# Kernel tuning notes

Measured on AMD Instinct MI355X. Metric: run time of the kernel, lower is better.

Reference implementation:

```python
import jax, jax.numpy as jnp
import numpy as np

D_MODEL = 1024
D_INNER = 2048   # expand * d_model
D_STATE = 16
D_CONV = 4
DT_RANK = 64     # ceil(d_model / 16)
BATCH = 2
SEQLEN = 4096


def setup_inputs() -> dict:
    key = jax.random.key(0)
    ks = jax.random.split(key, 9)
    g = lambda k, shape, scale: jax.random.normal(k, shape, dtype=jnp.float32) * scale
    hidden_states = g(ks[0], (BATCH, SEQLEN, D_MODEL), 1.0)
    W_in = g(ks[1], (2 * D_INNER, D_MODEL), D_MODEL ** -0.5)
    conv_w = g(ks[2], (D_INNER, D_CONV), D_CONV ** -0.5)
    conv_b = g(ks[3], (D_INNER,), 0.02)
    x_proj_w = g(ks[4], (DT_RANK + 2 * D_STATE, D_INNER), D_INNER ** -0.5)
    dt_w = g(ks[5], (D_INNER, DT_RANK), DT_RANK ** -0.5)
    # dt bias init as in Mamba: inverse softplus of dt ~ U[log(1e-3), log(1e-1)]
    dt = jnp.exp(jax.random.uniform(ks[6], (D_INNER,), dtype=jnp.float32)
                 * (np.log(0.1) - np.log(0.001)) + np.log(0.001))
    dt = jnp.clip(dt, 1e-4, None)
    dt_b = dt + jnp.log(-jnp.expm1(-dt))
    # A_log init: log of [1..d_state] repeated per channel
    A_log = jnp.log(jnp.tile(jnp.arange(1, D_STATE + 1, dtype=jnp.float32), (D_INNER, 1)))
    D = jnp.ones((D_INNER,), dtype=jnp.float32)
    W_out = g(ks[7], (D_MODEL, D_INNER), D_INNER ** -0.5)
    return dict(hidden_states=hidden_states, W_in=W_in, conv_w=conv_w, conv_b=conv_b,
                x_proj_w=x_proj_w, dt_w=dt_w, dt_b=dt_b, A_log=A_log, D=D, W_out=W_out)


def reference(hidden_states, W_in, conv_w, conv_b, x_proj_w, dt_w, dt_b, A_log, D, W_out):
    B, L, _ = hidden_states.shape
    # in_proj + transpose -> (B, 2*Din, L)
    xz = jnp.einsum('bld,ed->bel', hidden_states, W_in)
    # nanotron (tp=1) splits via view(B, d_inner, 2, L): interleaved channels
    xz = xz.reshape(B, D_INNER, 2, L)
    x, z = xz[:, :, 0, :], xz[:, :, 1, :]          # (B, Din, L)
    # causal depthwise conv1d (pad left d_conv-1) + SiLU
    xc = jax.lax.conv_general_dilated(
        x, conv_w[:, None, :], window_strides=(1,), padding=[(D_CONV - 1, 0)],
        dimension_numbers=('NCH', 'OIH', 'NCH'), feature_group_count=D_INNER)
    x = jax.nn.silu(xc + conv_b[None, :, None])     # (B, Din, L)
    # x_proj -> dt, B, C
    x_dbl = jnp.einsum('bdl,ed->ble', x, x_proj_w)  # (B, L, dt_rank+2N)
    dt, Bm, Cm = jnp.split(x_dbl, [DT_RANK, DT_RANK + D_STATE], axis=-1)
    delta = jnp.einsum('blr,dr->bdl', dt, dt_w)     # (B, Din, L)
    delta = jax.nn.softplus(delta + dt_b[None, :, None])
    A = -jnp.exp(A_log)                             # (Din, N)
    # selective scan over time
    xs = (jnp.transpose(delta, (2, 0, 1)),          # (L, B, Din)
          jnp.transpose(x, (2, 0, 1)),              # (L, B, Din)
          jnp.transpose(Bm, (1, 0, 2)),             # (L, B, N)
          jnp.transpose(Cm, (1, 0, 2)))             # (L, B, N)

    def step(s, inp):
        d_t, x_t, B_t, C_t = inp
        s = s * jnp.exp(d_t[:, :, None] * A[None]) + (d_t * x_t)[:, :, None] * B_t[:, None, :]
        y_t = jnp.einsum('bdn,bn->bd', s, C_t)
        return s, y_t

    s0 = jnp.zeros((B, D_INNER, D_STATE), dtype=hidden_states.dtype)
    _, ys = jax.lax.scan(step, s0, xs)              # ys: (L, B, Din)
    y = jnp.transpose(ys, (1, 2, 0))                # (B, Din, L)
    y = y + D[None, :, None] * x
    y = y * jax.nn.silu(z)
    out = jnp.einsum('bdl,md->blm', y, W_out)       # (B, L, d_model)
    return out
```

## Files before the change

kernel.cpp:

```cpp
#include <hip/hip_runtime.h>
#include <hip/hip_bf16.h>

#define D_MODEL 1024
#define D_INNER 2048
#define D_STATE 16
#define DT_RANK 64
#define BATCH 2
#define SEQLEN 4096
#define BL (BATCH * SEQLEN)
#define NPROJ (DT_RANK + 2 * D_STATE)
#define CH 64
#define NCH (SEQLEN / CH)

typedef __attribute__((ext_vector_type(8))) short bf16x8;
typedef __attribute__((ext_vector_type(4))) float f32x4;
struct S4 { short x, y, z, w; };

__device__ __forceinline__ float sigmoidf_(float v) {
    return 1.0f / (1.0f + __expf(-v));
}

__device__ __forceinline__ unsigned short bf16_rne(float f) {
    unsigned u = __float_as_uint(f);
    unsigned r = u + 0x7FFFu + ((u >> 16) & 1u);
    return (unsigned short)(r >> 16);
}

__device__ __forceinline__ float bf2f(short s) {
    return __uint_as_float(((unsigned)(unsigned short)s) << 16);
}

__global__ __launch_bounds__(256)
void cvt_split(const float* __restrict__ in, short* __restrict__ hi,
               short* __restrict__ lo, int n4) {
    const int i = blockIdx.x * 256 + threadIdx.x;
    if (i >= n4) return;
    const float4 v = reinterpret_cast<const float4*>(in)[i];
    const float f[4] = {v.x, v.y, v.z, v.w};
    S4 h, l;
    short hb[4], lb[4];
#pragma unroll
    for (int j = 0; j < 4; ++j) {
        const unsigned short hh = bf16_rne(f[j]);
        const float hf = __uint_as_float((unsigned)hh << 16);
        hb[j] = (short)hh;
        lb[j] = (short)bf16_rne(f[j] - hf);
    }
    h.x = hb[0]; h.y = hb[1]; h.z = hb[2]; h.w = hb[3];
    l.x = lb[0]; l.y = lb[1]; l.z = lb[2]; l.w = lb[3];
    *reinterpret_cast<S4*>(hi + (size_t)i * 4) = h;
    *reinterpret_cast<S4*>(lo + (size_t)i * 4) = l;
}

template <int EPI>
__global__ __launch_bounds__(256)
void gemm_bf16x3(const short* __restrict__ Ahi, const short* __restrict__ Alo,
                 const short* __restrict__ Bhi, const short* __restrict__ Blo,
                 float* __restrict__ C, int K, int lda, int ldb, int ldc,
                 const float* __restrict__ bias) {
    __shared__ short sA[2][2][128][32];
    __shared__ short sB[2][2][128][32];
    const int t = threadIdx.x;
    const int w = t >> 6, l = t & 63;

    const int nwg = gridDim.x * gridDim.y;
    int bid = blockIdx.y * gridDim.x + blockIdx.x;
    if ((nwg & 7) == 0) bid = (bid & 7) * (nwg >> 3) + (bid >> 3);
    const int m0 = (bid / gridDim.x) * 128, n0 = (bid % gridDim.x) * 128;
    const int wr = w >> 1, wc = w & 1;

    const short* gsrc;
    short* sd0;
    short* sd1;
    int ld, tile0;
    if (w == 0)      { gsrc = Ahi; sd0 = &sA[0][0][0][0]; sd1 = &sA[1][0][0][0]; tile0 = m0; ld = lda; }
    else if (w == 1) { gsrc = Alo; sd0 = &sA[0][1][0][0]; sd1 = &sA[1][1][0][0]; tile0 = m0; ld = lda; }
    else if (w == 2) { gsrc = Bhi; sd0 = &sB[0][0][0][0]; sd1 = &sB[1][0][0][0]; tile0 = n0; ld = ldb; }
    else             { gsrc = Blo; sd0 = &sB[0][1][0][0]; sd1 = &sB[1][1][0][0]; tile0 = n0; ld = ldb; }
    const int kc_src = ((l & 3) ^ ((l >> 3) & 3)) << 3;
    const size_t grow = (size_t)(tile0 + (l >> 2)) * ld + kc_src;

    f32x4 acc[4][4] = {};
    const int frow = l & 15;
    const int kb = (((l >> 4) ^ ((frow >> 1) & 3)) << 3);

    auto STAGE = [&](short* sdst, int k0) {
#pragma unroll
        for (int i = 0; i < 8; ++i) {
            const short* g = gsrc + grow + (size_t)(i << 4) * ld + k0;
            __builtin_amdgcn_global_load_lds(
                (const __attribute__((address_space(1))) void*)g,
                (__attribute__((address_space(3))) void*)(sdst + (i << 9)),
                16, 0, 0);
        }
    };

    auto COMPUTE = [&](int cur) {
        bf16x8 a[2][4], b[2][4];
#pragma unroll
        for (int f = 0; f < 4; ++f) {
            a[0][f] = *reinterpret_cast<const bf16x8*>(&sA[cur][0][wr * 64 + f * 16 + frow][kb]);
            a[1][f] = *reinterpret_cast<const bf16x8*>(&sA[cur][1][wr * 64 + f * 16 + frow][kb]);
            b[0][f] = *reinterpret_cast<const bf16x8*>(&sB[cur][0][wc * 64 + f * 16 + frow][kb]);
            b[1][f] = *reinterpret_cast<const bf16x8*>(&sB[cur][1][wc * 64 + f * 16 + frow][kb]);
        }
#pragma unroll
        for (int fi = 0; fi < 4; ++fi)
#pragma unroll
            for (int fj = 0; fj < 4; ++fj) {
                acc[fi][fj] = __builtin_amdgcn_mfma_f32_16x16x32_bf16(
                    a[0][fi], b[0][fj], acc[fi][fj], 0, 0, 0);
                acc[fi][fj] = __builtin_amdgcn_mfma_f32_16x16x32_bf16(
                    a[1][fi], b[0][fj], acc[fi][fj], 0, 0, 0);
                acc[fi][fj] = __builtin_amdgcn_mfma_f32_16x16x32_bf16(
                    a[0][fi], b[1][fj], acc[fi][fj], 0, 0, 0);
            }
    };

    const int NT = K >> 5;
    STAGE(sd0, 0);
    for (int tt = 0; tt < NT - 1; ++tt) {
        const int cur = tt & 1;
        STAGE(cur ? sd0 : sd1, (tt + 1) << 5);
        __builtin_amdgcn_sched_barrier(0);
        asm volatile("s_waitcnt vmcnt(8)" ::: "memory");
        __builtin_amdgcn_s_barrier();
        COMPUTE(cur);
        __builtin_amdgcn_sched_barrier(0);
        __builtin_amdgcn_s_barrier();
    }
    {
        const int cur = (NT - 1) & 1;
        __builtin_amdgcn_sched_barrier(0);
        asm volatile("s_waitcnt vmcnt(0)" ::: "memory");
        __builtin_amdgcn_s_barrier();
        COMPUTE(cur);
    }

    const int crow = (l >> 4) << 2;
    const int ccol = l & 15;
#pragma unroll
    for (int fi = 0; fi < 4; ++fi)
#pragma unroll
        for (int fj = 0; fj < 4; ++fj) {
            const int n = n0 + wc * 64 + fj * 16 + ccol;
#pragma unroll
            for (int r = 0; r < 4; ++r) {
                float v = acc[fi][fj][r];
                if (EPI == 1) {
                    v += bias[n];
                    v = fmaxf(v, 0.f) + log1pf(__expf(-fabsf(v)));
                }
                C[(size_t)(m0 + wr * 64 + fi * 16 + crow + r) * ldc + n] = v;
            }
        }
}

__global__ __launch_bounds__(256)
void gemm96(const short* __restrict__ Xhi, const short* __restrict__ Xlo,
            const short* __restrict__ Whi, const short* __restrict__ Wlo,
            float* __restrict__ C, short* __restrict__ dthi,
            short* __restrict__ dtlo) {
    const int t = threadIdx.x;
    const int w = t >> 6, l = t & 63;
    const int m0 = blockIdx.x * 32;
    const int rfrag = (w >> 1) * 16;
    const int cbase = (w & 1) * 48;
    const int lrow = l & 15;
    const int koff0 = (l >> 4) << 3;
    f32x4 acc[3] = {};
    const size_t arow = (size_t)(m0 + rfrag + lrow) * D_INNER;
#pragma unroll 2
    for (int k0 = 0; k0 < D_INNER; k0 += 32) {
        const int ko = k0 + koff0;
        const bf16x8 ah = *reinterpret_cast<const bf16x8*>(Xhi + arow + ko);
        const bf16x8 al = *reinterpret_cast<const bf16x8*>(Xlo + arow + ko);
#pragma unroll
        for (int jj = 0; jj < 3; ++jj) {
            const size_t brow = (size_t)(cbase + jj * 16 + lrow) * D_INNER + ko;
            const bf16x8 bh = *reinterpret_cast<const bf16x8*>(Whi + brow);
            const bf16x8 bl = *reinterpret_cast<const bf16x8*>(Wlo + brow);
            acc[jj] = __builtin_amdgcn_mfma_f32_16x16x32_bf16(ah, bh, acc[jj], 0, 0, 0);
            acc[jj] = __builtin_amdgcn_mfma_f32_16x16x32_bf16(al, bh, acc[jj], 0, 0, 0);
            acc[jj] = __builtin_amdgcn_mfma_f32_16x16x32_bf16(ah, bl, acc[jj], 0, 0, 0);
        }
    }
    const int crow = (l >> 4) << 2;
#pragma unroll
    for (int jj = 0; jj < 3; ++jj) {
        const int col = cbase + jj * 16 + lrow;
#pragma unroll
        for (int r = 0; r < 4; ++r) {
            const int m = m0 + rfrag + crow + r;
            const float v = acc[jj][r];
            C[(size_t)m * NPROJ + col] = v;
            if (col < DT_RANK) {
                const unsigned short hh = bf16_rne(v);
                dthi[(size_t)m * DT_RANK + col] = (short)hh;
                dtlo[(size_t)m * DT_RANK + col] =
                    (short)bf16_rne(v - __uint_as_float((unsigned)hh << 16));
            }
        }
    }
}

__global__ __launch_bounds__(256)
void conv_silu_k(const float* __restrict__ xr, const float* __restrict__ cw,
                 const float* __restrict__ cb, short* __restrict__ xchi,
                 short* __restrict__ xclo) {
    const int idx = blockIdx.x * 256 + threadIdx.x;
    const int d = idx & (D_INNER - 1);
    const int bl = idx >> 11;
    const int l = bl & (SEQLEN - 1);
    const float4 w4 = *reinterpret_cast<const float4*>(cw + (size_t)d * 4);
    const float wj[4] = {w4.x, w4.y, w4.z, w4.w};
    float acc = cb[d];
#pragma unroll
    for (int j = 0; j < 4; ++j) {
        const int ll = l - 3 + j;
        if (ll >= 0)
            acc += xr[(size_t)(bl - 3 + j) * D_INNER + d] * wj[j];
    }
    const float v = acc * sigmoidf_(acc);
    const unsigned short hh = bf16_rne(v);
    xchi[idx] = (short)hh;
    xclo[idx] = (short)bf16_rne(v - __uint_as_float((unsigned)hh << 16));
}

__global__ __launch_bounds__(256)
void scan1(const float* __restrict__ delta, const short* __restrict__ xchi,
           const short* __restrict__ xclo, const float* __restrict__ dtbc,
           const float* __restrict__ A_log, float* __restrict__ sum_delta,
           float* __restrict__ S_end) {
    const int d = blockIdx.x * 256 + threadIdx.x;
    const int b = blockIdx.y;
    const int c = blockIdx.z;
    __shared__ float bc[CH][32];
    for (int i = threadIdx.x; i < CH * 32; i += 256) {
        const int row = i >> 5, col = i & 31;
        bc[row][col] = dtbc[(size_t)(b * SEQLEN + c * CH + row) * NPROJ + DT_RANK + col];
    }
    __syncthreads();
    float A[16];
#pragma unroll
    for (int n = 0; n < 16; ++n) A[n] = -__expf(A_log[(size_t)d * 16 + n]);
    float s[16] = {0.f};
    float sd = 0.f;
    const size_t base = ((size_t)b * SEQLEN + (size_t)c * CH) * D_INNER + d;
    for (int li = 0; li < CH; ++li) {
        const size_t o = base + (size_t)li * D_INNER;
        const float dl = delta[o];
        const float xv = bf2f(xchi[o]) + bf2f(xclo[o]);
        sd += dl;
        const float dx = dl * xv;
#pragma unroll
        for (int n = 0; n < 16; ++n) {
            const float a = __expf(dl * A[n]);
            s[n] = fmaf(s[n], a, dx * bc[li][n]);
        }
    }
    sum_delta[((size_t)c * BATCH + b) * D_INNER + d] = sd;
#pragma unroll
    for (int n = 0; n < 16; ++n)
        S_end[(((size_t)c * BATCH + b) * 16 + n) * D_INNER + d] = s[n];
}

__global__ __launch_bounds__(256)
void scan2(const float* __restrict__ sum_delta, float* __restrict__ S,
           const float* __restrict__ A_log) {
    const int idx = blockIdx.x * 256 + threadIdx.x;
    const int d = idx & (D_INNER - 1);
    const int n = (idx >> 11) & 15;
    const int b = idx >> 15;
    const float A = -__expf(A_log[(size_t)d * 16 + n]);
    float carry = 0.f;
    for (int c = 0; c < NCH; ++c) {
        const float sd = sum_delta[((size_t)c * BATCH + b) * D_INNER + d];
        const size_t o = (((size_t)c * BATCH + b) * 16 + n) * D_INNER + d;
        const float se = S[o];
        S[o] = carry;
        carry = fmaf(carry, __expf(sd * A), se);
    }
}

__global__ __launch_bounds__(256)
void scan3(const float* __restrict__ delta, short* __restrict__ xchi,
           short* __restrict__ xclo, const float* __restrict__ z,
           const float* __restrict__ dtbc, const float* __restrict__ A_log,
           const float* __restrict__ S_init, const float* __restrict__ Dp) {
    const int d = blockIdx.x * 256 + threadIdx.x;
    const int b = blockIdx.y;
    const int c = blockIdx.z;
    __shared__ float bc[CH][32];
    for (int i = threadIdx.x; i < CH * 32; i += 256) {
        const int row = i >> 5, col = i & 31;
        bc[row][col] = dtbc[(size_t)(b * SEQLEN + c * CH + row) * NPROJ + DT_RANK + col];
    }
    __syncthreads();
    float A[16];
#pragma unroll
    for (int n = 0; n < 16; ++n) A[n] = -__expf(A_log[(size_t)d * 16 + n]);
    float s[16];
#pragma unroll
    for (int n = 0; n < 16; ++n)
        s[n] = S_init[(((size_t)c * BATCH + b) * 16 + n) * D_INNER + d];
    const float Dv = Dp[d];
    const size_t base = ((size_t)b * SEQLEN + (size_t)c * CH) * D_INNER + d;
    for (int li = 0; li < CH; ++li) {
        const size_t o = base + (size_t)li * D_INNER;
        const float dl = delta[o];
        const float xv = bf2f(xchi[o]) + bf2f(xclo[o]);
        const float dx = dl * xv;
        float y = 0.f;
#pragma unroll
        for (int n = 0; n < 16; ++n) {
            const float a = __expf(dl * A[n]);
            s[n] = fmaf(s[n], a, dx * bc[li][n]);
            y = fmaf(s[n], bc[li][16 + n], y);
        }
        const float zv = z[o];
        const float yv = (y + Dv * xv) * (zv * sigmoidf_(zv));
        const unsigned short hh = bf16_rne(yv);
        xchi[o] = (short)hh;
        xclo[o] = (short)bf16_rne(yv - __uint_as_float((unsigned)hh << 16));
    }
}

extern "C" void kernel_launch(void* const* d_in, const int* in_sizes, int n_in,
                              void* d_out, int out_size, void* d_ws, size_t ws_size,
                              hipStream_t stream) {
    const float* hidden   = (const float*)d_in[0];
    const float* W_in     = (const float*)d_in[1];
    const float* conv_w   = (const float*)d_in[2];
    const float* conv_b   = (const float*)d_in[3];
    const float* x_proj_w = (const float*)d_in[4];
    const float* dt_w     = (const float*)d_in[5];
    const float* dt_b     = (const float*)d_in[6];
    const float* A_log    = (const float*)d_in[7];
    const float* Dp       = (const float*)d_in[8];
    const float* W_out    = (const float*)d_in[9];
    float* out = (float*)d_out;

    float* ws    = (float*)d_ws;
    float* xbuf  = ws;
    float* zbuf  = xbuf + (size_t)BL * D_INNER;
    float* xcreg = zbuf + (size_t)BL * D_INNER;
    float* dtbc  = xcreg + (size_t)BL * D_INNER;
    float* sumd  = dtbc + (size_t)BL * NPROJ;
    float* Send  = sumd + (size_t)NCH * BATCH * D_INNER;

    short* xpwhi = (short*)(Send + (size_t)NCH * BATCH * 16 * D_INNER);
    short* xpwlo = xpwhi + (size_t)NPROJ * D_INNER;
    short* dtwhi = xpwlo + (size_t)NPROJ * D_INNER;
    short* dtwlo = dtwhi + (size_t)D_INNER * DT_RANK;
    short* dthi  = dtwlo + (size_t)D_INNER * DT_RANK;
    short* dtlo  = dthi + (size_t)BL * DT_RANK;

    short* hxhi  = (short*)xcreg;
    short* hxlo  = hxhi + (size_t)BL * D_MODEL;
    short* winhi = hxlo + (size_t)BL * D_MODEL;
    short* winlo = winhi + (size_t)2 * D_INNER * D_MODEL;

    const dim3 thr(256);

    cvt_split<<<dim3(BL * D_MODEL / 1024), thr, 0, stream>>>(hidden, hxhi, hxlo, BL * D_MODEL / 4);
    cvt_split<<<dim3(2 * D_INNER * D_MODEL / 1024), thr, 0, stream>>>(W_in, winhi, winlo, 2 * D_INNER * D_MODEL / 4);
    cvt_split<<<dim3(NPROJ * D_INNER / 1024), thr, 0, stream>>>(x_proj_w, xpwhi, xpwlo, NPROJ * D_INNER / 4);
    cvt_split<<<dim3(D_INNER * DT_RANK / 1024), thr, 0, stream>>>(dt_w, dtwhi, dtwlo, D_INNER * DT_RANK / 4);

    gemm_bf16x3<0><<<dim3(D_INNER / 128, BL / 128), thr, 0, stream>>>(
        hxhi, hxlo, winhi, winlo, xbuf, D_MODEL, D_MODEL, 2 * D_MODEL, D_INNER, nullptr);
    gemm_bf16x3<0><<<dim3(D_INNER / 128, BL / 128), thr, 0, stream>>>(
        hxhi, hxlo, winhi + D_MODEL, winlo + D_MODEL, zbuf, D_MODEL, D_MODEL, 2 * D_MODEL, D_INNER, nullptr);

    short* xchi = (short*)xcreg;
    short* xclo = xchi + (size_t)BL * D_INNER;
    conv_silu_k<<<dim3(BL * D_INNER / 256), thr, 0, stream>>>(xbuf, conv_w, conv_b, xchi, xclo);

    gemm96<<<dim3(BL / 32), thr, 0, stream>>>(xchi, xclo, xpwhi, xpwlo, dtbc, dthi, dtlo);

    gemm_bf16x3<1><<<dim3(D_INNER / 128, BL / 128), thr, 0, stream>>>(
        dthi, dtlo, dtwhi, dtwlo, xbuf, DT_RANK, DT_RANK, DT_RANK, D_INNER, dt_b);

    scan1<<<dim3(D_INNER / 256, BATCH, NCH), thr, 0, stream>>>(
        xbuf, xchi, xclo, dtbc, A_log, sumd, Send);
    scan2<<<dim3(BATCH * 16 * D_INNER / 256), thr, 0, stream>>>(sumd, Send, A_log);
    scan3<<<dim3(D_INNER / 256, BATCH, NCH), thr, 0, stream>>>(
        xbuf, xchi, xclo, zbuf, dtbc, A_log, Send, Dp);

    short* wohi = (short*)zbuf;
    short* wolo = wohi + (size_t)D_MODEL * D_INNER;
    cvt_split<<<dim3(D_MODEL * D_INNER / 1024), thr, 0, stream>>>(W_out, wohi, wolo, D_MODEL * D_INNER / 4);

    gemm_bf16x3<0><<<dim3(D_MODEL / 128, BL / 128), thr, 0, stream>>>(
        xchi, xclo, wohi, wolo, out, D_INNER, D_INNER, D_INNER, D_MODEL, nullptr);
}
```

Measured before the change: 709.4 us.

## Add 256x128-tile split-bf16 GEMM and merge in_proj x/z GEMMs into one launch

Introduces a 512-thread GEMM kernel with a 256x128 output tile, double-buffered async global-to-LDS staging and explicit waitcnt/barrier scheduling. It replaces the old 128x128 kernel for the input and output projections. The two in_proj GEMMs that read even and odd rows of W_in are fused into one launch over the full weight, with an epilogue that routes interleaved columns to the x and z buffers. The goal is more operand reuse per tile, fewer launches, and a single pass over the activations, at the cost of 96KB of LDS per block (lower occupancy) and strided, less coalesced stores in the split epilogue.

Measured after the change: 724.1 us. 2.1% more time.

```diff
diff --git a/kernel.cpp b/kernel.cpp
--- a/kernel.cpp
+++ b/kernel.cpp
@@ -30,6 +30,11 @@
     return __uint_as_float(((unsigned)(unsigned short)s) << 16);
 }
 
+#define GLOAD(gptr, dptr)                                              \
+    __builtin_amdgcn_global_load_lds(                                  \
+        (const __attribute__((address_space(1))) void*)(gptr),         \
+        (__attribute__((address_space(3))) void*)(dptr), 16, 0, 0)
+
 __global__ __launch_bounds__(256)
 void cvt_split(const float* __restrict__ in, short* __restrict__ hi,
                short* __restrict__ lo, int n4) {
@@ -50,6 +55,112 @@
     l.x = lb[0]; l.y = lb[1]; l.z = lb[2]; l.w = lb[3];
     *reinterpret_cast<S4*>(hi + (size_t)i * 4) = h;
     *reinterpret_cast<S4*>(lo + (size_t)i * 4) = l;
+}
+
+template <int EPI>
+__global__ __launch_bounds__(512)
+void gemm_bt256(const short* __restrict__ Ahi, const short* __restrict__ Alo,
+                const short* __restrict__ Bhi, const short* __restrict__ Blo,
+                float* __restrict__ C0, float* __restrict__ C1,
+                int K, int lda, int ldb, int ldc) {
+    extern __shared__ short smem[];
+    short* sA = smem;
+    short* sB = smem + 32768;
+    const int t = threadIdx.x;
+    const int w = t >> 6, l = t & 63;
+
+    const int nwg = gridDim.x * gridDim.y;
+    int bid = blockIdx.y * gridDim.x + blockIdx.x;
+    bid = (bid & 7) * (nwg >> 3) + (bid >> 3);
+    const int m0 = (bid / gridDim.x) * 256, n0 = (bid % gridDim.x) * 128;
+    const int wr = w >> 1, wc = w & 1;
+
+    const int r4 = l >> 2;
+    const int kc_src = ((l & 3) ^ ((l >> 3) & 3)) << 3;
+    const int frow = l & 15;
+    const int kb = (((l >> 4) ^ ((frow >> 1) & 3)) << 3);
+
+    f32x4 acc[4][4] = {};
+
+    auto STAGE = [&](int buf, int k0) {
+        const int sa0 = w, sa1 = 8 + w;
+        GLOAD(Ahi + (size_t)(m0 + sa0 * 16 + r4) * lda + k0 + kc_src,
+              sA + buf * 16384 + sa0 * 512);
+        GLOAD(Ahi + (size_t)(m0 + sa1 * 16 + r4) * lda + k0 + kc_src,
+              sA + buf * 16384 + sa1 * 512);
+        GLOAD(Alo + (size_t)(m0 + sa0 * 16 + r4) * lda + k0 + kc_src,
+              sA + buf * 16384 + 8192 + sa0 * 512);
+        GLOAD(Alo + (size_t)(m0 + sa1 * 16 + r4) * lda + k0 + kc_src,
+              sA + buf * 16384 + 8192 + sa1 * 512);
+        GLOAD(Bhi + (size_t)(n0 + w * 16 + r4) * ldb + k0 + kc_src,
+              sB + buf * 8192 + w * 512);
+        GLOAD(Blo + (size_t)(n0 + w * 16 + r4) * ldb + k0 + kc_src,
+              sB + buf * 8192 + 4096 + w * 512);
+    };
+
+    auto COMPUTE = [&](int buf) {
+        bf16x8 a[2][4], b[2][4];
+        const short* pA = sA + buf * 16384;
+        const short* pB = sB + buf * 8192;
+#pragma unroll
+        for (int f = 0; f < 4; ++f) {
+            a[0][f] = *reinterpret_cast<const bf16x8*>(&pA[(wr * 64 + f * 16 + frow) * 32 + kb]);
+            a[1][f] = *reinterpret_cast<const bf16x8*>(&pA[8192 + (wr * 64 + f * 16 + frow) * 32 + kb]);
+            b[0][f] = *reinterpret_cast<const bf16x8*>(&pB[(wc * 64 + f * 16 + frow) * 32 + kb]);
+            b[1][f] = *reinterpret_cast<const bf16x8*>(&pB[4096 + (wc * 64 + f * 16 + frow) * 32 + kb]);
+        }
+#pragma unroll
+        for (int fi = 0; fi < 4; ++fi)
+#pragma unroll
+            for (int fj = 0; fj < 4; ++fj) {
+                acc[fi][fj] = __builtin_amdgcn_mfma_f32_16x16x32_bf16(
+                    a[0][fi], b[0][fj], acc[fi][fj], 0, 0, 0);
+                acc[fi][fj] = __builtin_amdgcn_mfma_f32_16x16x32_bf16(
+                    a[1][fi], b[0][fj], acc[fi][fj], 0, 0, 0);
+                acc[fi][fj] = __builtin_amdgcn_mfma_f32_16x16x32_bf16(
+                    a[0][fi], b[1][fj], acc[fi][fj], 0, 0, 0);
+            }
+    };
+
+    const int NT = K >> 5;
+    STAGE(0, 0);
+    for (int tt = 0; tt < NT - 1; ++tt) {
+        const int cur = tt & 1;
+        STAGE(cur ^ 1, (tt + 1) << 5);
+        __builtin_amdgcn_sched_barrier(0);
+        asm volatile("s_waitcnt vmcnt(6)" ::: "memory");
+        __builtin_amdgcn_s_barrier();
+        COMPUTE(cur);
+        __builtin_amdgcn_sched_barrier(0);
+        __builtin_amdgcn_s_barrier();
+    }
+    {
+        const int cur = (NT - 1) & 1;
+        __builtin_amdgcn_sched_barrier(0);
+        asm volatile("s_waitcnt vmcnt(0)" ::: "memory");
+        __builtin_amdgcn_s_barrier();
+        COMPUTE(cur);
+    }
+
+    const int crow = (l >> 4) << 2;
+    const int ccol = l & 15;
+#pragma unroll
+    for (int fi = 0; fi < 4; ++fi)
+#pragma unroll
+        for (int fj = 0; fj < 4; ++fj) {
+            const int n = n0 + wc * 64 + fj * 16 + ccol;
+#pragma unroll
+            for (int r = 0; r < 4; ++r) {
+                const float v = acc[fi][fj][r];
+                const size_t row = (size_t)(m0 + wr * 64 + fi * 16 + crow + r);
+                if (EPI == 2) {
+                    float* dst = (n & 1) ? C1 : C0;
+                    dst[row * ldc + (n >> 1)] = v;
+                } else {
+                    C0[row * ldc + n] = v;
+                }
+            }
+        }
 }
 
 template <int EPI>
@@ -88,10 +199,7 @@
 #pragma unroll
         for (int i = 0; i < 8; ++i) {
             const short* g = gsrc + grow + (size_t)(i << 4) * ld + k0;
-            __builtin_amdgcn_global_load_lds(
-                (const __attribute__((address_space(1))) void*)g,
-                (__attribute__((address_space(3))) void*)(sdst + (i << 9)),
-                16, 0, 0);
+            GLOAD(g, sdst + (i << 9));
         }
     };
 
@@ -368,10 +476,8 @@
     cvt_split<<<dim3(NPROJ * D_INNER / 1024), thr, 0, stream>>>(x_proj_w, xpwhi, xpwlo, NPROJ * D_INNER / 4);
     cvt_split<<<dim3(D_INNER * DT_RANK / 1024), thr, 0, stream>>>(dt_w, dtwhi, dtwlo, D_INNER * DT_RANK / 4);
 
-    gemm_bf16x3<0><<<dim3(D_INNER / 128, BL / 128), thr, 0, stream>>>(
-        hxhi, hxlo, winhi, winlo, xbuf, D_MODEL, D_MODEL, 2 * D_MODEL, D_INNER, nullptr);
-    gemm_bf16x3<0><<<dim3(D_INNER / 128, BL / 128), thr, 0, stream>>>(
-        hxhi, hxlo, winhi + D_MODEL, winlo + D_MODEL, zbuf, D_MODEL, D_MODEL, 2 * D_MODEL, D_INNER, nullptr);
+    gemm_bt256<2><<<dim3(2 * D_INNER / 128, BL / 256), dim3(512), 98304, stream>>>(
+        hxhi, hxlo, winhi, winlo, xbuf, zbuf, D_MODEL, D_MODEL, D_MODEL, D_INNER);
 
     short* xchi = (short*)xcreg;
     short* xclo = xchi + (size_t)BL * D_INNER;
@@ -392,6 +498,6 @@
     short* wolo = wohi + (size_t)D_MODEL * D_INNER;
     cvt_split<<<dim3(D_MODEL * D_INNER / 1024), thr, 0, stream>>>(W_out, wohi, wolo, D_MODEL * D_INNER / 4);
 
-    gemm_bf16x3<0><<<dim3(D_MODEL / 128, BL / 128), thr, 0, stream>>>(
-        xchi, xclo, wohi, wolo, out, D_INNER, D_INNER, D_INNER, D_MODEL, nullptr);
-}
+    gemm_bt256<0><<<dim3(D_MODEL / 128, BL / 256), dim3(512), 98304, stream>>>(
+        xchi, xclo, wohi, wolo, out, nullptr, D_INNER, D_INNER, D_INNER, D_MODEL);
+}
```
